# Kernel tuning notes

Measured on AMD Instinct MI355X. Metric: run time of the kernel, lower is better.

Reference implementation:

```python
import jax, jax.numpy as jnp
import numpy as np

N = 50000   # nodes
E = 800000  # edges
F = 2       # num_feats
D = 2       # output_dim
H = 64      # hidden_size
L = 2       # num_layers
T = 12      # seq_len
HZN = 12    # horizon
NEG_SLOPE = 0.2


def setup_inputs() -> dict:
    key = jax.random.key(0)
    ks = jax.random.split(key, 10)
    x = jax.random.normal(ks[0], (T, N, F), dtype=jnp.float32)
    src = jax.random.randint(ks[1], (E,), 0, N, dtype=jnp.int32)
    dst = jax.random.randint(ks[2], (E,), 0, N, dtype=jnp.int32)

    def conv_params(k, fin):
        k1, k2, k3 = jax.random.split(k, 3)
        s = 1.0 / np.sqrt(fin)
        W = (jax.random.normal(k1, (3, fin, H), jnp.float32) * s)
        al = (jax.random.normal(k2, (3, H), jnp.float32) * s)
        ar = (jax.random.normal(k3, (3, H), jnp.float32) * s)
        b = jnp.zeros((3, H), jnp.float32)
        return W, al, ar, b

    enc_W0, enc_al0, enc_ar0, enc_b0 = conv_params(ks[3], F + H)
    enc_W1, enc_al1, enc_ar1, enc_b1 = conv_params(ks[4], 2 * H)
    dec_W0, dec_al0, dec_ar0, dec_b0 = conv_params(ks[5], D + H)
    dec_W1, dec_al1, dec_ar1, dec_b1 = conv_params(ks[6], 2 * H)
    proj_W = jax.random.normal(ks[7], (H, D), jnp.float32) / np.sqrt(H)
    proj_b = jnp.zeros((D,), jnp.float32)
    return dict(x=x, src=src, dst=dst,
                enc_W0=enc_W0, enc_al0=enc_al0, enc_ar0=enc_ar0, enc_b0=enc_b0,
                enc_W1=enc_W1, enc_al1=enc_al1, enc_ar1=enc_ar1, enc_b1=enc_b1,
                dec_W0=dec_W0, dec_al0=dec_al0, dec_ar0=dec_ar0, dec_b0=dec_b0,
                dec_W1=dec_W1, dec_al1=dec_al1, dec_ar1=dec_ar1, dec_b1=dec_b1,
                proj_W=proj_W, proj_b=proj_b)


def _gat(feat, W, al, ar, b, src, dst):
    # DGL GATConv, single head: fc -> edge attention -> edge softmax -> aggregate.
    h = feat @ W                              # [N, H]
    el = (h * al).sum(-1)                     # [N] source attention logits
    er = (h * ar).sum(-1)                     # [N] destination attention logits
    e = jax.nn.leaky_relu(el[src] + er[dst], NEG_SLOPE)   # [E]
    m = jax.ops.segment_max(e, dst, num_segments=N)       # per-dst max (stable softmax)
    ex = jnp.exp(e - m[dst])                               # [E]
    s = jax.ops.segment_sum(ex, dst, num_segments=N)       # [N]
    alpha = ex / jnp.maximum(s[dst], 1e-9)                 # [E] edge softmax
    out = jax.ops.segment_sum(h[src] * alpha[:, None], dst, num_segments=N)  # [N, H]
    return out + b


def _gru(xin, hx, W, al, ar, b, src, dst):
    iv = jnp.concatenate([xin, hx], axis=1)
    r = jax.nn.sigmoid(_gat(iv, W[0], al[0], ar[0], b[0], src, dst))
    z = jax.nn.sigmoid(_gat(iv, W[1], al[1], ar[1], b[1], src, dst))
    hc = jnp.tanh(_gat(jnp.concatenate([xin, r * hx], axis=1), W[2], al[2], ar[2], b[2], src, dst))
    return z * hx + (1.0 - z) * hc


def reference(x, src, dst,
              enc_W0, enc_al0, enc_ar0, enc_b0,
              enc_W1, enc_al1, enc_ar1, enc_b1,
              dec_W0, dec_al0, dec_ar0, dec_b0,
              dec_W1, dec_al1, dec_ar1, dec_b1,
              proj_W, proj_b):
    enc_params = [(enc_W0, enc_al0, enc_ar0, enc_b0), (enc_W1, enc_al1, enc_ar1, enc_b1)]
    dec_params = [(dec_W0, dec_al0, dec_ar0, dec_b0), (dec_W1, dec_al1, dec_ar1, dec_b1)]

    def enc_step(hstack, xt):
        out = xt
        new = []
        for i, (W, al, ar, b) in enumerate(enc_params):
            hn = _gru(out, hstack[i], W, al, ar, b, src, dst)
            new.append(hn)
            out = hn
        return jnp.stack(new), None

    h0 = jnp.zeros((L, N, H), x.dtype)
    hT, _ = jax.lax.scan(enc_step, h0, x)

    def dec_step(carry, _):
        dec_in, hstack = carry
        out = dec_in
        new = []
        for i, (W, al, ar, b) in enumerate(dec_params):
            hn = _gru(out, hstack[i], W, al, ar, b, src, dst)
            new.append(hn)
            out = hn
        pred = out @ proj_W + proj_b                 # [N, D]
        return (pred, jnp.stack(new)), pred

    dec_in0 = jnp.zeros((N, D), x.dtype)
    _, outputs = jax.lax.scan(dec_step, (dec_in0, hT), None, length=HZN)
    return outputs  # [horizon, N, output_dim]
```

## Files before the change

### kernel.cpp

```cpp
#include <hip/hip_runtime.h>
#include <hip/hip_bf16.h>

__device__ __forceinline__ float wsum64(float v) {
#pragma unroll
  for (int m = 32; m > 0; m >>= 1) v += __shfl_xor(v, m, 64);
  return v;
}
__device__ __forceinline__ float gsum16(float v) {
#pragma unroll
  for (int m = 8; m > 0; m >>= 1) v += __shfl_xor(v, m, 16);
  return v;
}
__device__ __forceinline__ float lrelu(float x) { return x > 0.f ? x : 0.2f * x; }
__device__ __forceinline__ float sigf(float x) { return 1.f / (1.f + __expf(-x)); }

__global__ void hist_k(const int* __restrict__ dst, int* __restrict__ cnt, int e) {
  int i = blockIdx.x * blockDim.x + threadIdx.x;
  if (i < e) atomicAdd(&cnt[dst[i]], 1);
}

__global__ __launch_bounds__(256) void bsum_k(const int* __restrict__ cnt,
                                              int* __restrict__ bsum, int n) {
  __shared__ int red[4];
  int base = blockIdx.x * 1024;
  int t = threadIdx.x;
  int v = 0;
#pragma unroll
  for (int i = 0; i < 4; i++) {
    int idx = base + t + i * 256;
    v += (idx < n) ? cnt[idx] : 0;
  }
#pragma unroll
  for (int m = 32; m > 0; m >>= 1) v += __shfl_xor(v, m, 64);
  if ((t & 63) == 0) red[t >> 6] = v;
  __syncthreads();
  if (t == 0) bsum[blockIdx.x] = red[0] + red[1] + red[2] + red[3];
}

__global__ __launch_bounds__(1024) void scan_bsum_k(int* __restrict__ bsum,
                                                    int* __restrict__ rpn, int nb) {
  __shared__ int buf[1024];
  int t = threadIdx.x;
  int v = (t < nb) ? bsum[t] : 0;
  buf[t] = v;
  __syncthreads();
  int val = v;
  for (int off = 1; off < 1024; off <<= 1) {
    int u = (t >= off) ? buf[t - off] : 0;
    __syncthreads();
    val += u;
    buf[t] = val;
    __syncthreads();
  }
  if (t < nb) bsum[t] = val - v;
  if (t == nb - 1) *rpn = val;
}

__global__ __launch_bounds__(1024) void scan_fin_k(const int* __restrict__ cnt,
                                                   const int* __restrict__ bsum,
                                                   int* __restrict__ rp,
                                                   int* __restrict__ cursor, int n) {
  __shared__ int buf[1024];
  int t = threadIdx.x;
  int idx = blockIdx.x * 1024 + t;
  int v = (idx < n) ? cnt[idx] : 0;
  buf[t] = v;
  __syncthreads();
  int val = v;
  for (int off = 1; off < 1024; off <<= 1) {
    int u = (t >= off) ? buf[t - off] : 0;
    __syncthreads();
    val += u;
    buf[t] = val;
    __syncthreads();
  }
  if (idx < n) {
    int e = bsum[blockIdx.x] + val - v;
    rp[idx] = e;
    cursor[idx] = e;
  }
}

__global__ void scatter_k(const int* __restrict__ src, const int* __restrict__ dst,
                          int* __restrict__ cursor, int* __restrict__ srcs, int e) {
  int i = blockIdx.x * blockDim.x + threadIdx.x;
  if (i < e) {
    int pos = atomicAdd(&cursor[dst[i]], 1);
    srcs[pos] = src[i];
  }
}

template <int FA, int NG>
__global__ __launch_bounds__(512) void mm_k(
    const float* __restrict__ xa, const float* __restrict__ xb,
    const float* __restrict__ Wg,
    const float* __restrict__ al, const float* __restrict__ ar,
    float* __restrict__ hb, float* __restrict__ el, float* __restrict__ er, int n) {
  constexpr int KP = FA + 64;
  __shared__ float Wl[KP * 64 * NG];
  __shared__ float Xl[32 * KP];
  for (int i = threadIdx.x; i < KP * 64; i += 512) {
    if (NG == 2) {
      float2 wv = {Wg[i], Wg[(size_t)KP * 64 + i]};
      *(float2*)&Wl[i * 2] = wv;
    } else {
      Wl[i] = Wg[i];
    }
  }
  int rbase = blockIdx.x * 32;
  for (int i = threadIdx.x; i < 32 * KP; i += 512) {
    int row = i / KP, k = i - row * KP;
    int r = rbase + row; if (r >= n) r = n - 1;
    Xl[i] = (k < FA) ? xa[(size_t)r * FA + k] : xb[(size_t)r * 64 + (k - FA)];
  }
  __syncthreads();
  int lane = threadIdx.x & 63, w = threadIdx.x >> 6;
  int rb = rbase + w * 4;
  if (rb >= n) return;
  float a_l[NG], a_r[NG];
#pragma unroll
  for (int g = 0; g < NG; g++) { a_l[g] = al[g * 64 + lane]; a_r[g] = ar[g * 64 + lane]; }
  float acc[4][NG];
#pragma unroll
  for (int i = 0; i < 4; i++)
#pragma unroll
    for (int g = 0; g < NG; g++) acc[i][g] = 0.f;
  const int xoff = (w * 4) * KP;
#pragma unroll 8
  for (int k = 0; k < KP; k += 2) {
    float2 w0, w1;
    if (NG == 2) {
      w0 = *(const float2*)&Wl[(k * 64 + lane) * 2];
      w1 = *(const float2*)&Wl[((k + 1) * 64 + lane) * 2];
    } else {
      w0.x = Wl[k * 64 + lane]; w0.y = 0.f;
      w1.x = Wl[(k + 1) * 64 + lane]; w1.y = 0.f;
    }
#pragma unroll
    for (int i = 0; i < 4; i++) {
      float2 xv = *(const float2*)&Xl[xoff + i * KP + k];
      acc[i][0] = fmaf(xv.x, w0.x, acc[i][0]);
      acc[i][0] = fmaf(xv.y, w1.x, acc[i][0]);
      if (NG == 2) {
        acc[i][1] = fmaf(xv.x, w0.y, acc[i][1]);
        acc[i][1] = fmaf(xv.y, w1.y, acc[i][1]);
      }
    }
  }
#pragma unroll
  for (int i = 0; i < 4; i++) {
    int r = rb + i;
    bool ok = r < n;
#pragma unroll
    for (int g = 0; g < NG; g++) {
      if (ok) hb[(size_t)r * (64 * NG) + g * 64 + lane] = acc[i][g];
      float sl = wsum64(acc[i][g] * a_l[g]);
      float sr = wsum64(acc[i][g] * a_r[g]);
      if (ok && lane == 0) {
        el[(size_t)r * NG + g] = sl;
        er[(size_t)r * NG + g] = sr;
      }
    }
  }
}

__global__ __launch_bounds__(256) void agg_rz_k(
    const int* __restrict__ rp, const int* __restrict__ srcs,
    const float* __restrict__ hbuf, const float* __restrict__ elrz, const float* __restrict__ errz,
    const float* __restrict__ b,
    const float* __restrict__ hx, float* __restrict__ rh, float* __restrict__ zb, int n) {
  int l16 = threadIdx.x & 15;
  int d = (blockIdx.x * 256 + threadIdx.x) >> 4;
  if (d >= n) return;
  int beg = rp[d], deg = rp[d + 1] - beg;
  float2 erd = ((const float2*)errz)[d];
  const float4* h4 = (const float4*)hbuf;
  float4 accr = {0, 0, 0, 0}, accz = {0, 0, 0, 0};
  float sr = 0.f, sz = 0.f;
  for (int base = 0; base < deg; base += 16) {
    int k = base + l16;
    int s = 0;
    float exr = 0.f, exz = 0.f;
    if (k < deg) {
      s = srcs[beg + k];
      float2 el = ((const float2*)elrz)[s];
      exr = __expf(lrelu(el.x + erd.x));
      exz = __expf(lrelu(el.y + erd.y));
      sr += exr; sz += exz;
    }
#pragma unroll
    for (int j = 0; j < 16; j++) {
      int sj = __shfl(s, j, 16);
      float aj = __shfl(exr, j, 16);
      float zj = __shfl(exz, j, 16);
      float4 hr = h4[(size_t)sj * 32 + l16];
      float4 hz = h4[(size_t)sj * 32 + 16 + l16];
      accr.x = fmaf(aj, hr.x, accr.x); accr.y = fmaf(aj, hr.y, accr.y);
      accr.z = fmaf(aj, hr.z, accr.z); accr.w = fmaf(aj, hr.w, accr.w);
      accz.x = fmaf(zj, hz.x, accz.x); accz.y = fmaf(zj, hz.y, accz.y);
      accz.z = fmaf(zj, hz.z, accz.z); accz.w = fmaf(zj, hz.w, accz.w);
    }
  }
  sr = gsum16(sr); sz = gsum16(sz);
  float invr = 1.f / fmaxf(sr, 1e-9f);
  float invz = 1.f / fmaxf(sz, 1e-9f);
  float4 br4 = ((const float4*)b)[l16];
  float4 bz4 = ((const float4*)(b + 64))[l16];
  float4 hx4 = ((const float4*)hx)[(size_t)d * 16 + l16];
  float4 rv, zv;
  rv.x = sigf(fmaf(accr.x, invr, br4.x)) * hx4.x;
  rv.y = sigf(fmaf(accr.y, invr, br4.y)) * hx4.y;
  rv.z = sigf(fmaf(accr.z, invr, br4.z)) * hx4.z;
  rv.w = sigf(fmaf(accr.w, invr, br4.w)) * hx4.w;
  zv.x = sigf(fmaf(accz.x, invz, bz4.x));
  zv.y = sigf(fmaf(accz.y, invz, bz4.y));
  zv.z = sigf(fmaf(accz.z, invz, bz4.z));
  zv.w = sigf(fmaf(accz.w, invz, bz4.w));
  ((float4*)rh)[(size_t)d * 16 + l16] = rv;
  ((float4*)zb)[(size_t)d * 16 + l16] = zv;
}

__global__ __launch_bounds__(256) void agg_c_k(
    const int* __restrict__ rp, const int* __restrict__ srcs,
    const float* __restrict__ hc, const float* __restrict__ elc, const float* __restrict__ erc,
    const float* __restrict__ b, const float* __restrict__ zb, float* __restrict__ hstate,
    const float* __restrict__ projW, const float* __restrict__ projb,
    float* __restrict__ outp, int n) {
  int l16 = threadIdx.x & 15;
  int d = (blockIdx.x * 256 + threadIdx.x) >> 4;
  if (d >= n) return;
  int beg = rp[d], deg = rp[d + 1] - beg;
  float erd = erc[d];
  const float4* h4 = (const float4*)hc;
  float4 acc = {0, 0, 0, 0};
  float ssum = 0.f;
  for (int base = 0; base < deg; base += 16) {
    int k = base + l16;
    int s = 0;
    float ex = 0.f;
    if (k < deg) {
      s = srcs[beg + k];
      ex = __expf(lrelu(elc[s] + erd));
      ssum += ex;
    }
#pragma unroll
    for (int j = 0; j < 16; j++) {
      int sj = __shfl(s, j, 16);
      float aj = __shfl(ex, j, 16);
      float4 hv = h4[(size_t)sj * 16 + l16];
      acc.x = fmaf(aj, hv.x, acc.x); acc.y = fmaf(aj, hv.y, acc.y);
      acc.z = fmaf(aj, hv.z, acc.z); acc.w = fmaf(aj, hv.w, acc.w);
    }
  }
  ssum = gsum16(ssum);
  float inv = 1.f / fmaxf(ssum, 1e-9f);
  float4 bc4 = ((const float4*)b)[l16];
  float4 z4 = ((const float4*)zb)[(size_t)d * 16 + l16];
  float4 hx4 = ((const float4*)hstate)[(size_t)d * 16 + l16];
  float4 hcv, hn;
  hcv.x = tanhf(fmaf(acc.x, inv, bc4.x));
  hcv.y = tanhf(fmaf(acc.y, inv, bc4.y));
  hcv.z = tanhf(fmaf(acc.z, inv, bc4.z));
  hcv.w = tanhf(fmaf(acc.w, inv, bc4.w));
  hn.x = z4.x * hx4.x + (1.f - z4.x) * hcv.x;
  hn.y = z4.y * hx4.y + (1.f - z4.y) * hcv.y;
  hn.z = z4.z * hx4.z + (1.f - z4.z) * hcv.z;
  hn.w = z4.w * hx4.w + (1.f - z4.w) * hcv.w;
  ((float4*)hstate)[(size_t)d * 16 + l16] = hn;
  if (outp) {
    const float4* wp4 = (const float4*)projW;
    float4 a0 = wp4[l16 * 2], a1 = wp4[l16 * 2 + 1];
    float p0 = hn.x * a0.x + hn.y * a0.z + hn.z * a1.x + hn.w * a1.z;
    float p1 = hn.x * a0.y + hn.y * a0.w + hn.z * a1.y + hn.w * a1.w;
    p0 = gsum16(p0); p1 = gsum16(p1);
    if (l16 == 0) {
      outp[(size_t)d * 2 + 0] = p0 + projb[0];
      outp[(size_t)d * 2 + 1] = p1 + projb[1];
    }
  }
}

extern "C" void kernel_launch(void* const* d_in, const int* in_sizes, int n_in,
                              void* d_out, int out_size, void* d_ws, size_t ws_size,
                              hipStream_t stream) {
  const int T = 12, HZN = 12, F = 2, H = 64;
  const float* x = (const float*)d_in[0];
  const int* src = (const int*)d_in[1];
  const int* dst = (const int*)d_in[2];
  const float* enc_W0 = (const float*)d_in[3];
  const float* enc_al0 = (const float*)d_in[4];
  const float* enc_ar0 = (const float*)d_in[5];
  const float* enc_b0 = (const float*)d_in[6];
  const float* enc_W1 = (const float*)d_in[7];
  const float* enc_al1 = (const float*)d_in[8];
  const float* enc_ar1 = (const float*)d_in[9];
  const float* enc_b1 = (const float*)d_in[10];
  const float* dec_W0 = (const float*)d_in[11];
  const float* dec_al0 = (const float*)d_in[12];
  const float* dec_ar0 = (const float*)d_in[13];
  const float* dec_b0 = (const float*)d_in[14];
  const float* dec_W1 = (const float*)d_in[15];
  const float* dec_al1 = (const float*)d_in[16];
  const float* dec_ar1 = (const float*)d_in[17];
  const float* dec_b1 = (const float*)d_in[18];
  const float* proj_W = (const float*)d_in[19];
  const float* proj_b = (const float*)d_in[20];
  float* out = (float*)d_out;

  const int E = in_sizes[1];
  const int N = in_sizes[0] / (T * F);
  const int NB = (N + 1023) / 1024;

  char* wp = (char*)d_ws;
  size_t off = 0;
  auto carve = [&](size_t bytes) {
    void* p = wp + off;
    off = (off + bytes + 255) & ~(size_t)255;
    return p;
  };
  int* counts = (int*)carve((size_t)N * 4);
  int* bsum = (int*)carve((size_t)NB * 4);
  int* rp = (int*)carve((size_t)(N + 1) * 4);
  int* cursor = (int*)carve((size_t)N * 4);
  int* srcs = (int*)carve((size_t)E * 4);
  float* hs0 = (float*)carve((size_t)N * H * 4);
  float* hs1 = (float*)carve((size_t)N * H * 4);
  float* hbuf = (float*)carve((size_t)N * 2 * H * 4);
  float* elrz = (float*)carve((size_t)N * 2 * 4);
  float* errz = (float*)carve((size_t)N * 2 * 4);
  float* hc = (float*)carve((size_t)N * H * 4);
  float* elc = (float*)carve((size_t)N * 4);
  float* erc = (float*)carve((size_t)N * 4);
  float* rh = (float*)carve((size_t)N * H * 4);
  float* zbuf = (float*)carve((size_t)N * H * 4);
  float* zero2 = (float*)carve((size_t)N * F * 4);
  (void)ws_size;

  const int G_E = (E + 255) / 256;
  const int G_MM = (N + 31) / 32;
  const int G_AG = (N + 15) / 16;

  hipMemsetAsync(counts, 0, (size_t)N * 4, stream);
  hist_k<<<G_E, 256, 0, stream>>>(dst, counts, E);
  bsum_k<<<NB, 256, 0, stream>>>(counts, bsum, N);
  scan_bsum_k<<<1, 1024, 0, stream>>>(bsum, rp + N, NB);
  scan_fin_k<<<NB, 1024, 0, stream>>>(counts, bsum, rp, cursor, N);
  scatter_k<<<G_E, 256, 0, stream>>>(src, dst, cursor, srcs, E);

  hipMemsetAsync(hs0, 0, (size_t)N * H * 4, stream);
  hipMemsetAsync(hs1, 0, (size_t)N * H * 4, stream);
  hipMemsetAsync(zero2, 0, (size_t)N * F * 4, stream);

  auto run_gru = [&](const float* xa, int FA, float* hstate,
                     const float* W, const float* al, const float* ar, const float* b,
                     float* outp) {
    int fin = FA + H;
    if (FA == 2) {
      mm_k<2, 2><<<G_MM, 512, 0, stream>>>(xa, hstate, W, al, ar, hbuf, elrz, errz, N);
    } else {
      mm_k<64, 2><<<G_MM, 512, 0, stream>>>(xa, hstate, W, al, ar, hbuf, elrz, errz, N);
    }
    agg_rz_k<<<G_AG, 256, 0, stream>>>(rp, srcs, hbuf, elrz, errz, b, hstate, rh, zbuf, N);
    if (FA == 2) {
      mm_k<2, 1><<<G_MM, 512, 0, stream>>>(xa, rh, W + (size_t)2 * fin * H, al + 128, ar + 128,
                                           hc, elc, erc, N);
    } else {
      mm_k<64, 1><<<G_MM, 512, 0, stream>>>(xa, rh, W + (size_t)2 * fin * H, al + 128, ar + 128,
                                            hc, elc, erc, N);
    }
    agg_c_k<<<G_AG, 256, 0, stream>>>(rp, srcs, hc, elc, erc, b + 128, zbuf, hstate,
                                      proj_W, proj_b, outp, N);
  };

  for (int t = 0; t < T; t++) {
    const float* xt = x + (size_t)t * N * F;
    run_gru(xt, 2, hs0, enc_W0, enc_al0, enc_ar0, enc_b0, nullptr);
    run_gru(hs0, 64, hs1, enc_W1, enc_al1, enc_ar1, enc_b1, nullptr);
  }

  for (int t = 0; t < HZN; t++) {
    const float* xin = (t == 0) ? zero2 : (out + (size_t)(t - 1) * N * 2);
    run_gru(xin, 2, hs0, dec_W0, dec_al0, dec_ar0, dec_b0, nullptr);
    run_gru(hs0, 64, hs1, dec_W1, dec_al1, dec_ar1, dec_b1, out + (size_t)t * N * 2);
  }
  (void)out_size; (void)n_in;
}
```

Before: 8.196 ms.

## Fuse GEMM projections into graph aggregation kernels across GRU steps

Removes the standalone matmul launches: the candidate-gate projection of r*h is computed inside the r/z aggregation kernel, and the next cell's r/z projection is computed inside the candidate aggregation kernel. This drops the rh intermediate buffer and halves the kernel launches per GRU cell, cutting global memory round trips. In exchange, each block reloads the full weight matrix into shared memory, the matmul now runs on 16-lane groups with shuffles instead of the tiled form, and the higher shared-memory footprint may lower occupancy for the gather-heavy aggregation.

```diff
diff --git a/kernel.cpp b/kernel.cpp
--- a/kernel.cpp
+++ b/kernel.cpp
@@ -13,6 +13,32 @@
 }
 __device__ __forceinline__ float lrelu(float x) { return x > 0.f ? x : 0.2f * x; }
 __device__ __forceinline__ float sigf(float x) { return 1.f / (1.f + __expf(-x)); }
+__device__ __forceinline__ float dp4(float4 a, float4 b) {
+  return a.x * b.x + a.y * b.y + a.z * b.z + a.w * b.w;
+}
+
+#define MM1(f, row)                                        \
+  {                                                        \
+    float4 w_ = W4[(row) * 16 + l16];                      \
+    acc.x = fmaf((f), w_.x, acc.x);                        \
+    acc.y = fmaf((f), w_.y, acc.y);                        \
+    acc.z = fmaf((f), w_.z, acc.z);                        \
+    acc.w = fmaf((f), w_.w, acc.w);                        \
+  }
+
+#define MM2(f, row)                                        \
+  {                                                        \
+    float4 wr_ = W4[(row) * 32 + l16];                     \
+    float4 wz_ = W4[(row) * 32 + 16 + l16];                \
+    aR.x = fmaf((f), wr_.x, aR.x);                         \
+    aR.y = fmaf((f), wr_.y, aR.y);                         \
+    aR.z = fmaf((f), wr_.z, aR.z);                         \
+    aR.w = fmaf((f), wr_.w, aR.w);                         \
+    aZ.x = fmaf((f), wz_.x, aZ.x);                         \
+    aZ.y = fmaf((f), wz_.y, aZ.y);                         \
+    aZ.z = fmaf((f), wz_.z, aZ.z);                         \
+    aZ.w = fmaf((f), wz_.w, aZ.w);                         \
+  }
 
 __global__ void hist_k(const int* __restrict__ dst, int* __restrict__ cnt, int e) {
   int i = blockIdx.x * blockDim.x + threadIdx.x;
@@ -90,22 +116,17 @@
   }
 }
 
-template <int FA, int NG>
-__global__ __launch_bounds__(512) void mm_k(
+template <int FA>
+__global__ __launch_bounds__(512) void mm0_k(
     const float* __restrict__ xa, const float* __restrict__ xb,
-    const float* __restrict__ Wg,
-    const float* __restrict__ al, const float* __restrict__ ar,
+    const float* __restrict__ Wg, const float* __restrict__ al, const float* __restrict__ ar,
     float* __restrict__ hb, float* __restrict__ el, float* __restrict__ er, int n) {
   constexpr int KP = FA + 64;
-  __shared__ float Wl[KP * 64 * NG];
+  __shared__ float Wl[KP * 128];
   __shared__ float Xl[32 * KP];
   for (int i = threadIdx.x; i < KP * 64; i += 512) {
-    if (NG == 2) {
-      float2 wv = {Wg[i], Wg[(size_t)KP * 64 + i]};
-      *(float2*)&Wl[i * 2] = wv;
-    } else {
-      Wl[i] = Wg[i];
-    }
+    float2 wv = {Wg[i], Wg[(size_t)KP * 64 + i]};
+    *(float2*)&Wl[i * 2] = wv;
   }
   int rbase = blockIdx.x * 32;
   for (int i = threadIdx.x; i < 32 * KP; i += 512) {
@@ -117,60 +138,66 @@
   int lane = threadIdx.x & 63, w = threadIdx.x >> 6;
   int rb = rbase + w * 4;
   if (rb >= n) return;
-  float a_l[NG], a_r[NG];
-#pragma unroll
-  for (int g = 0; g < NG; g++) { a_l[g] = al[g * 64 + lane]; a_r[g] = ar[g * 64 + lane]; }
-  float acc[4][NG];
-#pragma unroll
-  for (int i = 0; i < 4; i++)
-#pragma unroll
-    for (int g = 0; g < NG; g++) acc[i][g] = 0.f;
+  float alr = al[lane], arr_ = ar[lane];
+  float alz = al[64 + lane], arz = ar[64 + lane];
+  float accr[4], accz[4];
+#pragma unroll
+  for (int i = 0; i < 4; i++) { accr[i] = 0.f; accz[i] = 0.f; }
   const int xoff = (w * 4) * KP;
 #pragma unroll 8
   for (int k = 0; k < KP; k += 2) {
-    float2 w0, w1;
-    if (NG == 2) {
-      w0 = *(const float2*)&Wl[(k * 64 + lane) * 2];
-      w1 = *(const float2*)&Wl[((k + 1) * 64 + lane) * 2];
-    } else {
-      w0.x = Wl[k * 64 + lane]; w0.y = 0.f;
-      w1.x = Wl[(k + 1) * 64 + lane]; w1.y = 0.f;
-    }
+    float2 w0 = *(const float2*)&Wl[(k * 64 + lane) * 2];
+    float2 w1 = *(const float2*)&Wl[((k + 1) * 64 + lane) * 2];
 #pragma unroll
     for (int i = 0; i < 4; i++) {
       float2 xv = *(const float2*)&Xl[xoff + i * KP + k];
-      acc[i][0] = fmaf(xv.x, w0.x, acc[i][0]);
-      acc[i][0] = fmaf(xv.y, w1.x, acc[i][0]);
-      if (NG == 2) {
-        acc[i][1] = fmaf(xv.x, w0.y, acc[i][1]);
-        acc[i][1] = fmaf(xv.y, w1.y, acc[i][1]);
-      }
+      accr[i] = fmaf(xv.x, w0.x, accr[i]);
+      accz[i] = fmaf(xv.x, w0.y, accz[i]);
+      accr[i] = fmaf(xv.y, w1.x, accr[i]);
+      accz[i] = fmaf(xv.y, w1.y, accz[i]);
     }
   }
 #pragma unroll
   for (int i = 0; i < 4; i++) {
     int r = rb + i;
     bool ok = r < n;
-#pragma unroll
-    for (int g = 0; g < NG; g++) {
-      if (ok) hb[(size_t)r * (64 * NG) + g * 64 + lane] = acc[i][g];
-      float sl = wsum64(acc[i][g] * a_l[g]);
-      float sr = wsum64(acc[i][g] * a_r[g]);
-      if (ok && lane == 0) {
-        el[(size_t)r * NG + g] = sl;
-        er[(size_t)r * NG + g] = sr;
-      }
-    }
-  }
-}
-
-__global__ __launch_bounds__(256) void agg_rz_k(
+    if (ok) {
+      hb[(size_t)r * 128 + lane] = accr[i];
+      hb[(size_t)r * 128 + 64 + lane] = accz[i];
+    }
+    float s0 = wsum64(accr[i] * alr);
+    float s1 = wsum64(accz[i] * alz);
+    float s2 = wsum64(accr[i] * arr_);
+    float s3 = wsum64(accz[i] * arz);
+    if (ok && lane == 0) {
+      el[(size_t)r * 2 + 0] = s0;
+      el[(size_t)r * 2 + 1] = s1;
+      er[(size_t)r * 2 + 0] = s2;
+      er[(size_t)r * 2 + 1] = s3;
+    }
+  }
+}
+
+template <int FA>
+__global__ __launch_bounds__(512) void kb_k(
     const int* __restrict__ rp, const int* __restrict__ srcs,
-    const float* __restrict__ hbuf, const float* __restrict__ elrz, const float* __restrict__ errz,
-    const float* __restrict__ b,
-    const float* __restrict__ hx, float* __restrict__ rh, float* __restrict__ zb, int n) {
+    const float* __restrict__ hbuf, const float* __restrict__ elrz,
+    const float* __restrict__ errz, const float* __restrict__ b,
+    const float* __restrict__ xa, const float* __restrict__ hx,
+    const float* __restrict__ Wc, const float* __restrict__ alc,
+    const float* __restrict__ arc,
+    float* __restrict__ hc, float* __restrict__ elc, float* __restrict__ erc,
+    float* __restrict__ zb, int n) {
+  constexpr int KP = FA + 64;
+  __shared__ float WlC[KP * 64];
+  for (int i = threadIdx.x; i < KP * 64; i += 512) {
+    int k = i >> 6, c = i & 63;
+    int ks = (k < 64) ? (FA + k) : (k - 64);
+    WlC[i] = Wc[(size_t)ks * 64 + c];
+  }
+  __syncthreads();
   int l16 = threadIdx.x & 15;
-  int d = (blockIdx.x * 256 + threadIdx.x) >> 4;
+  int d = blockIdx.x * 32 + (threadIdx.x >> 4);
   if (d >= n) return;
   int beg = rp[d], deg = rp[d + 1] - beg;
   float2 erd = ((const float2*)errz)[d];
@@ -216,18 +243,68 @@
   zv.y = sigf(fmaf(accz.y, invz, bz4.y));
   zv.z = sigf(fmaf(accz.z, invz, bz4.z));
   zv.w = sigf(fmaf(accz.w, invz, bz4.w));
-  ((float4*)rh)[(size_t)d * 16 + l16] = rv;
   ((float4*)zb)[(size_t)d * 16 + l16] = zv;
-}
-
-__global__ __launch_bounds__(256) void agg_c_k(
+  const float4* W4 = (const float4*)WlC;
+  float4 acc = {0, 0, 0, 0};
+#pragma unroll
+  for (int o = 0; o < 16; o++) {
+    float f0 = __shfl(rv.x, o, 16);
+    float f1 = __shfl(rv.y, o, 16);
+    float f2 = __shfl(rv.z, o, 16);
+    float f3 = __shfl(rv.w, o, 16);
+    MM1(f0, 4 * o + 0); MM1(f1, 4 * o + 1);
+    MM1(f2, 4 * o + 2); MM1(f3, 4 * o + 3);
+  }
+  if (FA == 2) {
+    float f0 = xa[(size_t)d * 2 + 0];
+    float f1 = xa[(size_t)d * 2 + 1];
+    MM1(f0, 64); MM1(f1, 65);
+  } else {
+    float4 xv = ((const float4*)xa)[(size_t)d * 16 + l16];
+#pragma unroll
+    for (int o = 0; o < 16; o++) {
+      float f0 = __shfl(xv.x, o, 16);
+      float f1 = __shfl(xv.y, o, 16);
+      float f2 = __shfl(xv.z, o, 16);
+      float f3 = __shfl(xv.w, o, 16);
+      MM1(f0, 64 + 4 * o + 0); MM1(f1, 64 + 4 * o + 1);
+      MM1(f2, 64 + 4 * o + 2); MM1(f3, 64 + 4 * o + 3);
+    }
+  }
+  float4 alv = ((const float4*)alc)[l16];
+  float4 arv = ((const float4*)arc)[l16];
+  float sl = gsum16(dp4(acc, alv));
+  float sr2 = gsum16(dp4(acc, arv));
+  if (l16 == 0) { elc[d] = sl; erc[d] = sr2; }
+  ((float4*)hc)[(size_t)d * 16 + l16] = acc;
+}
+
+template <int FAN, bool NEXT>
+__global__ __launch_bounds__(512) void kc_k(
     const int* __restrict__ rp, const int* __restrict__ srcs,
-    const float* __restrict__ hc, const float* __restrict__ elc, const float* __restrict__ erc,
-    const float* __restrict__ b, const float* __restrict__ zb, float* __restrict__ hstate,
+    const float* __restrict__ hc, const float* __restrict__ elc,
+    const float* __restrict__ erc, const float* __restrict__ bc,
+    const float* __restrict__ zb, float* __restrict__ hstate,
     const float* __restrict__ projW, const float* __restrict__ projb,
-    float* __restrict__ outp, int n) {
+    float* __restrict__ outp,
+    const float* __restrict__ Wn, const float* __restrict__ aln,
+    const float* __restrict__ arn, const float* __restrict__ xan,
+    const float* __restrict__ hxn,
+    float* __restrict__ hbn, float* __restrict__ elrzn, float* __restrict__ errzn,
+    int n) {
+  constexpr int KPN = FAN + 64;
+  __shared__ float WlN[NEXT ? KPN * 128 : 1];
+  if constexpr (NEXT) {
+    for (int i = threadIdx.x; i < KPN * 128; i += 512) {
+      int k = i >> 7, gc = i & 127;
+      int g = gc >> 6, c = gc & 63;
+      int ks = (k < 64) ? (FAN + k) : (k - 64);
+      WlN[i] = Wn[((size_t)g * KPN + ks) * 64 + c];
+    }
+    __syncthreads();
+  }
   int l16 = threadIdx.x & 15;
-  int d = (blockIdx.x * 256 + threadIdx.x) >> 4;
+  int d = blockIdx.x * 32 + (threadIdx.x >> 4);
   if (d >= n) return;
   int beg = rp[d], deg = rp[d + 1] - beg;
   float erd = erc[d];
@@ -254,7 +331,7 @@
   }
   ssum = gsum16(ssum);
   float inv = 1.f / fmaxf(ssum, 1e-9f);
-  float4 bc4 = ((const float4*)b)[l16];
+  float4 bc4 = ((const float4*)bc)[l16];
   float4 z4 = ((const float4*)zb)[(size_t)d * 16 + l16];
   float4 hx4 = ((const float4*)hstate)[(size_t)d * 16 + l16];
   float4 hcv, hn;
@@ -267,42 +344,81 @@
   hn.z = z4.z * hx4.z + (1.f - z4.z) * hcv.z;
   hn.w = z4.w * hx4.w + (1.f - z4.w) * hcv.w;
   ((float4*)hstate)[(size_t)d * 16 + l16] = hn;
+  float p0 = 0.f, p1 = 0.f;
   if (outp) {
     const float4* wp4 = (const float4*)projW;
     float4 a0 = wp4[l16 * 2], a1 = wp4[l16 * 2 + 1];
-    float p0 = hn.x * a0.x + hn.y * a0.z + hn.z * a1.x + hn.w * a1.z;
-    float p1 = hn.x * a0.y + hn.y * a0.w + hn.z * a1.y + hn.w * a1.w;
-    p0 = gsum16(p0); p1 = gsum16(p1);
+    p0 = gsum16(hn.x * a0.x + hn.y * a0.z + hn.z * a1.x + hn.w * a1.z) + projb[0];
+    p1 = gsum16(hn.x * a0.y + hn.y * a0.w + hn.z * a1.y + hn.w * a1.w) + projb[1];
     if (l16 == 0) {
-      outp[(size_t)d * 2 + 0] = p0 + projb[0];
-      outp[(size_t)d * 2 + 1] = p1 + projb[1];
-    }
+      outp[(size_t)d * 2 + 0] = p0;
+      outp[(size_t)d * 2 + 1] = p1;
+    }
+  }
+  if constexpr (NEXT) {
+    const float4* W4 = (const float4*)WlN;
+    float4 hxn4 = ((const float4*)hxn)[(size_t)d * 16 + l16];
+    float4 aR = {0, 0, 0, 0}, aZ = {0, 0, 0, 0};
+#pragma unroll
+    for (int o = 0; o < 16; o++) {
+      float f0 = __shfl(hxn4.x, o, 16);
+      float f1 = __shfl(hxn4.y, o, 16);
+      float f2 = __shfl(hxn4.z, o, 16);
+      float f3 = __shfl(hxn4.w, o, 16);
+      MM2(f0, 4 * o + 0); MM2(f1, 4 * o + 1);
+      MM2(f2, 4 * o + 2); MM2(f3, 4 * o + 3);
+    }
+    if (FAN == 2) {
+      float f0, f1;
+      if (xan) { f0 = xan[(size_t)d * 2 + 0]; f1 = xan[(size_t)d * 2 + 1]; }
+      else { f0 = p0; f1 = p1; }
+      MM2(f0, 64); MM2(f1, 65);
+    } else {
+      float4 xv = xan ? ((const float4*)xan)[(size_t)d * 16 + l16] : hn;
+#pragma unroll
+      for (int o = 0; o < 16; o++) {
+        float f0 = __shfl(xv.x, o, 16);
+        float f1 = __shfl(xv.y, o, 16);
+        float f2 = __shfl(xv.z, o, 16);
+        float f3 = __shfl(xv.w, o, 16);
+        MM2(f0, 64 + 4 * o + 0); MM2(f1, 64 + 4 * o + 1);
+        MM2(f2, 64 + 4 * o + 2); MM2(f3, 64 + 4 * o + 3);
+      }
+    }
+    float4 alr4 = ((const float4*)aln)[l16];
+    float4 alz4 = ((const float4*)(aln + 64))[l16];
+    float4 arr4 = ((const float4*)arn)[l16];
+    float4 arz4 = ((const float4*)(arn + 64))[l16];
+    float e0 = gsum16(dp4(aR, alr4));
+    float e1 = gsum16(dp4(aZ, alz4));
+    float e2 = gsum16(dp4(aR, arr4));
+    float e3 = gsum16(dp4(aZ, arz4));
+    if (l16 == 0) {
+      elrzn[(size_t)d * 2 + 0] = e0;
+      elrzn[(size_t)d * 2 + 1] = e1;
+      errzn[(size_t)d * 2 + 0] = e2;
+      errzn[(size_t)d * 2 + 1] = e3;
+    }
+    ((float4*)hbn)[(size_t)d * 32 + l16] = aR;
+    ((float4*)hbn)[(size_t)d * 32 + 16 + l16] = aZ;
   }
 }
 
 extern "C" void kernel_launch(void* const* d_in, const int* in_sizes, int n_in,
                               void* d_out, int out_size, void* d_ws, size_t ws_size,
                               hipStream_t stream) {
-  const int T = 12, HZN = 12, F = 2, H = 64;
+  const int T = 12, F = 2, H = 64;
   const float* x = (const float*)d_in[0];
   const int* src = (const int*)d_in[1];
   const int* dst = (const int*)d_in[2];
-  const float* enc_W0 = (const float*)d_in[3];
-  const float* enc_al0 = (const float*)d_in[4];
-  const float* enc_ar0 = (const float*)d_in[5];
-  const float* enc_b0 = (const float*)d_in[6];
-  const float* enc_W1 = (const float*)d_in[7];
-  const float* enc_al1 = (const float*)d_in[8];
-  const float* enc_ar1 = (const float*)d_in[9];
-  const float* enc_b1 = (const float*)d_in[10];
-  const float* dec_W0 = (const float*)d_in[11];
-  const float* dec_al0 = (const float*)d_in[12];
-  const float* dec_ar0 = (const float*)d_in[13];
-  const float* dec_b0 = (const float*)d_in[14];
-  const float* dec_W1 = (const float*)d_in[15];
-  const float* dec_al1 = (const float*)d_in[16];
-  const float* dec_ar1 = (const float*)d_in[17];
-  const float* dec_b1 = (const float*)d_in[18];
+  const float* Ws[4] = {(const float*)d_in[3], (const float*)d_in[7],
+                        (const float*)d_in[11], (const float*)d_in[15]};
+  const float* als[4] = {(const float*)d_in[4], (const float*)d_in[8],
+                         (const float*)d_in[12], (const float*)d_in[16]};
+  const float* ars[4] = {(const float*)d_in[5], (const float*)d_in[9],
+                         (const float*)d_in[13], (const float*)d_in[17]};
+  const float* bs[4] = {(const float*)d_in[6], (const float*)d_in[10],
+                        (const float*)d_in[14], (const float*)d_in[18]};
   const float* proj_W = (const float*)d_in[19];
   const float* proj_b = (const float*)d_in[20];
   float* out = (float*)d_out;
@@ -328,17 +444,15 @@
   float* hbuf = (float*)carve((size_t)N * 2 * H * 4);
   float* elrz = (float*)carve((size_t)N * 2 * 4);
   float* errz = (float*)carve((size_t)N * 2 * 4);
-  float* hc = (float*)carve((size_t)N * H * 4);
+  float* hcb = (float*)carve((size_t)N * H * 4);
   float* elc = (float*)carve((size_t)N * 4);
   float* erc = (float*)carve((size_t)N * 4);
-  float* rh = (float*)carve((size_t)N * H * 4);
   float* zbuf = (float*)carve((size_t)N * H * 4);
   float* zero2 = (float*)carve((size_t)N * F * 4);
   (void)ws_size;
 
   const int G_E = (E + 255) / 256;
-  const int G_MM = (N + 31) / 32;
-  const int G_AG = (N + 15) / 16;
+  const int G32 = (N + 31) / 32;
 
   hipMemsetAsync(counts, 0, (size_t)N * 4, stream);
   hist_k<<<G_E, 256, 0, stream>>>(dst, counts, E);
@@ -351,37 +465,61 @@
   hipMemsetAsync(hs1, 0, (size_t)N * H * 4, stream);
   hipMemsetAsync(zero2, 0, (size_t)N * F * 4, stream);
 
-  auto run_gru = [&](const float* xa, int FA, float* hstate,
-                     const float* W, const float* al, const float* ar, const float* b,
-                     float* outp) {
-    int fin = FA + H;
-    if (FA == 2) {
-      mm_k<2, 2><<<G_MM, 512, 0, stream>>>(xa, hstate, W, al, ar, hbuf, elrz, errz, N);
+  mm0_k<2><<<G32, 512, 0, stream>>>(x, hs0, Ws[0], als[0], ars[0], hbuf, elrz, errz, N);
+
+  for (int i = 0; i < 48; i++) {
+    bool enc = i < 24;
+    int j = enc ? i : i - 24;
+    int t = j >> 1, layer = j & 1;
+    int type = (enc ? 0 : 2) + layer;
+    const float* W = Ws[type];
+    const float* al = als[type];
+    const float* ar = ars[type];
+    const float* b = bs[type];
+    int FA = layer ? 64 : 2;
+    size_t KP = FA + 64;
+    const float* Wc = W + (size_t)2 * KP * 64;
+    const float* xa = layer ? hs0
+                            : (enc ? x + (size_t)t * N * 2
+                                   : (t == 0 ? zero2 : out + (size_t)(t - 1) * N * 2));
+    float* hstate = layer ? hs1 : hs0;
+    float* outp = (!enc && layer) ? out + (size_t)t * N * 2 : nullptr;
+
+    if (FA == 2)
+      kb_k<2><<<G32, 512, 0, stream>>>(rp, srcs, hbuf, elrz, errz, b, xa, hstate,
+                                       Wc, al + 128, ar + 128, hcb, elc, erc, zbuf, N);
+    else
+      kb_k<64><<<G32, 512, 0, stream>>>(rp, srcs, hbuf, elrz, errz, b, xa, hstate,
+                                        Wc, al + 128, ar + 128, hcb, elc, erc, zbuf, N);
+
+    if (i == 47) {
+      kc_k<2, false><<<G32, 512, 0, stream>>>(
+          rp, srcs, hcb, elc, erc, b + 128, zbuf, hstate, proj_W, proj_b, outp,
+          nullptr, nullptr, nullptr, nullptr, nullptr, nullptr, nullptr, nullptr, N);
     } else {
-      mm_k<64, 2><<<G_MM, 512, 0, stream>>>(xa, hstate, W, al, ar, hbuf, elrz, errz, N);
-    }
-    agg_rz_k<<<G_AG, 256, 0, stream>>>(rp, srcs, hbuf, elrz, errz, b, hstate, rh, zbuf, N);
-    if (FA == 2) {
-      mm_k<2, 1><<<G_MM, 512, 0, stream>>>(xa, rh, W + (size_t)2 * fin * H, al + 128, ar + 128,
-                                           hc, elc, erc, N);
-    } else {
-      mm_k<64, 1><<<G_MM, 512, 0, stream>>>(xa, rh, W + (size_t)2 * fin * H, al + 128, ar + 128,
-                                            hc, elc, erc, N);
-    }
-    agg_c_k<<<G_AG, 256, 0, stream>>>(rp, srcs, hc, elc, erc, b + 128, zbuf, hstate,
-                                      proj_W, proj_b, outp, N);
-  };
-
-  for (int t = 0; t < T; t++) {
-    const float* xt = x + (size_t)t * N * F;
-    run_gru(xt, 2, hs0, enc_W0, enc_al0, enc_ar0, enc_b0, nullptr);
-    run_gru(hs0, 64, hs1, enc_W1, enc_al1, enc_ar1, enc_b1, nullptr);
-  }
-
-  for (int t = 0; t < HZN; t++) {
-    const float* xin = (t == 0) ? zero2 : (out + (size_t)(t - 1) * N * 2);
-    run_gru(xin, 2, hs0, dec_W0, dec_al0, dec_ar0, dec_b0, nullptr);
-    run_gru(hs0, 64, hs1, dec_W1, dec_al1, dec_ar1, dec_b1, out + (size_t)t * N * 2);
+      int i2 = i + 1;
+      bool enc2 = i2 < 24;
+      int j2 = enc2 ? i2 : i2 - 24;
+      int t2 = j2 >> 1, l2 = j2 & 1;
+      int type2 = (enc2 ? 0 : 2) + l2;
+      const float* Wn = Ws[type2];
+      const float* aln = als[type2];
+      const float* arn = ars[type2];
+      const float* xan = nullptr;
+      if (l2 == 0) {
+        if (enc2) xan = x + (size_t)t2 * N * 2;
+        else if (t2 == 0) xan = zero2;
+      }
+      float* hxn = l2 ? hs1 : hs0;
+      if (l2)
+        kc_k<64, true><<<G32, 512, 0, stream>>>(
+            rp, srcs, hcb, elc, erc, b + 128, zbuf, hstate, proj_W, proj_b, outp,
+            Wn, aln, arn, xan, hxn, hbuf, elrz, errz, N);
+      else
+        kc_k<2, true><<<G32, 512, 0, stream>>>(
+            rp, srcs, hcb, elc, erc, b + 128, zbuf, hstate, proj_W, proj_b, outp,
+            Wn, aln, arn, xan, hxn, hbuf, elrz, errz, N);
+    }
   }
   (void)out_size; (void)n_in;
 }
```

Measured after the change: 30.60 ms. 273% more time.
